# Kernel tuning notes

Measured on AMD Instinct MI355X. Metric: run time of the kernel, lower is better.

## Reference

```python
import jax, jax.numpy as jnp
import numpy as np

EMBED = 1024
HEADS = 16
HEAD_DIM = EMBED // HEADS


def setup_inputs() -> dict:
    key = jax.random.key(0)
    ks = jax.random.split(key, 6)
    s = 1.0 / np.sqrt(EMBED)
    return {
        "x": jax.random.normal(ks[0], (4, 4096, EMBED), dtype=jnp.float32),
        "Wq": jax.random.normal(ks[1], (EMBED, EMBED), dtype=jnp.float32) * s,
        "Wk": jax.random.normal(ks[2], (EMBED, EMBED), dtype=jnp.float32) * s,
        "Wv": jax.random.normal(ks[3], (EMBED, EMBED), dtype=jnp.float32) * s,
        "Wo": jax.random.normal(ks[4], (EMBED, EMBED), dtype=jnp.float32) * s,
        "bo": jax.random.normal(ks[5], (EMBED,), dtype=jnp.float32) * 0.01,
    }


def reference(x, Wq, Wk, Wv, Wo, bo):
    # Faithful to the torch module, including its cross-head attention:
    # the einsum subscripts in the original treat the HEAD axis as the
    # attended (q/k) axis and the SEQUENCE axis as a batch axis.
    N, L, E = x.shape
    H, D = HEADS, HEAD_DIM
    q = (x @ Wq).reshape(N, L, H, D)
    k = (x @ Wk).reshape(N, L, H, D)
    v = (x @ Wv).reshape(N, L, H, D)
    # energy[n, l, hq, hk] = sum_d q[n, l, hq, d] * k[n, l, hk, d]
    energy = jnp.einsum('nlqd,nlkd->nlqk', q, k)  # (N, L, H, H)
    scale = jnp.asarray(E, x.dtype) ** 0.5
    attn = jax.nn.softmax(energy / scale, axis=-1)
    out = jnp.einsum('nlqk,nlkd->nlqd', attn, v).reshape(N, L, E)
    return out @ Wo + bo
```

## Files before the change

### kernel.cpp

```cpp
#include <hip/hip_runtime.h>


typedef unsigned short u16;
typedef unsigned int u32;

typedef __bf16 bf16x8 __attribute__((ext_vector_type(8)));
typedef float f32x4 __attribute__((ext_vector_type(4)));

__device__ __forceinline__ u16 f2bf(float f) {
  u32 u = __float_as_uint(f);
  u += 0x7fffu + ((u >> 16) & 1u);
  return (u16)(u >> 16);
}
__device__ __forceinline__ float bflo(u32 u) { return __uint_as_float(u << 16); }
__device__ __forceinline__ float bfhi(u32 u) { return __uint_as_float(u & 0xffff0000u); }

__device__ __forceinline__ void load_lds16(const u16* g, u16* l) {
  __builtin_amdgcn_global_load_lds(
      (const __attribute__((address_space(1))) u32*)g,
      (__attribute__((address_space(3))) u32*)l, 16, 0, 0);
}

__global__ __launch_bounds__(256) void prep_kernel(
    const float* __restrict__ x, u16* __restrict__ xb,
    const float* __restrict__ Wq, const float* __restrict__ Wk,
    const float* __restrict__ Wv, const float* __restrict__ Wo,
    u16* __restrict__ Wt, u16* __restrict__ Wot) {
  const int bid = blockIdx.x, tid = threadIdx.x;
  if (bid < 8192) {
    size_t i = (size_t)bid * 256 + tid;
    const float4* p = (const float4*)x;
    float4 a = p[2 * i], b = p[2 * i + 1];
    u32 w0 = (u32)f2bf(a.x) | ((u32)f2bf(a.y) << 16);
    u32 w1 = (u32)f2bf(a.z) | ((u32)f2bf(a.w) << 16);
    u32 w2 = (u32)f2bf(b.x) | ((u32)f2bf(b.y) << 16);
    u32 w3 = (u32)f2bf(b.z) | ((u32)f2bf(b.w) << 16);
    *(uint4*)(xb + 8 * i) = make_uint4(w0, w1, w2, w3);
  } else {
    __shared__ float tile[32][33];
    const int b = bid - 8192;
    const int z = b >> 10, rem = b & 1023;
    const float* W = (z == 0) ? Wq : (z == 1) ? Wk : (z == 2) ? Wv : Wo;
    u16* D = (z < 3) ? (Wt + (size_t)z * 1024 * 1024) : Wot;
    const int n0 = (rem & 31) * 32, k0 = (rem >> 5) * 32;
    const int tx = tid & 31, ty = tid >> 5;
#pragma unroll
    for (int i = 0; i < 4; i++)
      tile[ty + i * 8][tx] = W[(size_t)(k0 + ty + i * 8) * 1024 + n0 + tx];
    __syncthreads();
#pragma unroll
    for (int i = 0; i < 4; i++)
      D[(size_t)(n0 + ty + i * 8) * 1024 + k0 + tx] = f2bf(tile[tx][ty + i * 8]);
  }
}


#define SYNC_IN()                                      \
  __builtin_amdgcn_s_barrier();                        \
  asm volatile("s_waitcnt lgkmcnt(0)" ::: "memory");   \
  __builtin_amdgcn_sched_barrier(0)

#define MM(FM, FN, Af, Bf)                                                      \
  do {                                                                          \
    __builtin_amdgcn_s_setprio(1);                                              \
    _Pragma("unroll") for (int m_ = 0; m_ < 4; m_++)                            \
    _Pragma("unroll") for (int j_ = 0; j_ < 2; j_++)                            \
    _Pragma("unroll") for (int k_ = 0; k_ < 2; k_++)                            \
        acc[(FM) + m_][(FN) + j_] = __builtin_amdgcn_mfma_f32_16x16x32_bf16(    \
            Af[m_][k_], Bf[j_][k_], acc[(FM) + m_][(FN) + j_], 0, 0, 0);        \
    __builtin_amdgcn_s_setprio(0);                                              \
  } while (0)

template <int WRITE_MODE>
__global__ __launch_bounds__(512, 2) void gemm8(const u16* __restrict__ A,
                                                const u16* __restrict__ Bt,
                                                void* __restrict__ Cv,
                                                const float* __restrict__ bias,
                                                int N, int K) {
  extern __shared__ __align__(16) u16 smem[];
  const int t = threadIdx.x;
  const int lane = t & 63;
  const int wave = t >> 6;
  const int wm = wave >> 2;
  const int wn = wave & 3;
  const int lrow = lane & 15, lq = lane >> 4;
  const int wm64 = wm * 64, wn32 = wn * 32;

  const int bid = blockIdx.x;
  const int bm_t = ((bid & 7) << 3) | ((bid >> 3) & 7);
  const int bn_t = bid >> 6;
  const size_t bm = (size_t)bm_t * 256;
  const size_t bn = (size_t)bn_t * 256;

  const u16* Ap = A + bm * K;
  const u16* Bp = Bt + bn * K;
  const size_t halfK = (size_t)128 * K;
  const int NT = K >> 6;

  int srow[2], soff[2], sdst[2];
#pragma unroll
  for (int i = 0; i < 2; i++) {
    const int s = (i << 9) + t;
    srow[i] = s >> 3;
    soff[i] = ((s & 7) ^ (srow[i] & 7)) << 3;
    sdst[i] = s << 3;
  }

#define RG(buf, op, h) (smem + ((((buf) << 2) | ((op) << 1) | (h)) << 13))

  auto STG = [&](const u16* Gp, int kt, u16* L) {
#pragma unroll
    for (int i = 0; i < 2; i++)
      load_lds16(Gp + (size_t)srow[i] * K + (kt << 6) + soff[i], L + sdst[i]);
  };
  auto LDA = [&](bf16x8 (&f)[4][2], const u16* base) {
#pragma unroll
    for (int m = 0; m < 4; m++) {
      const int rh = wm64 + m * 16 + lrow;
      const int ro = rh << 6, rx = rh & 7;
#pragma unroll
      for (int ks = 0; ks < 2; ks++)
        f[m][ks] = *(const bf16x8*)&base[ro + ((((ks << 2) + lq) ^ rx) << 3)];
    }
  };
  auto LDB = [&](bf16x8 (&f)[2][2], const u16* base) {
#pragma unroll
    for (int j = 0; j < 2; j++) {
      const int ch = wn32 + j * 16 + lrow;
      const int co = ch << 6, cx = ch & 7;
#pragma unroll
      for (int ks = 0; ks < 2; ks++)
        f[j][ks] = *(const bf16x8*)&base[co + ((((ks << 2) + lq) ^ cx) << 3)];
    }
  };

  f32x4 acc[8][4];
#pragma unroll
  for (int i = 0; i < 8; i++)
#pragma unroll
    for (int j = 0; j < 4; j++) acc[i][j] = 0.0f;

  bf16x8 af[4][2], bf0[2][2], bf1[2][2];

  STG(Ap, 0, RG(0, 0, 0));
  STG(Bp, 0, RG(0, 1, 0));
  STG(Bp + halfK, 0, RG(0, 1, 1));
  STG(Ap + halfK, 0, RG(0, 0, 1));
  STG(Ap, 1, RG(1, 0, 0));
  STG(Bp, 1, RG(1, 1, 0));
  STG(Bp + halfK, 1, RG(1, 1, 1));
  asm volatile("s_waitcnt vmcnt(0)" ::: "memory");
  __builtin_amdgcn_s_barrier();

  for (int tt = 0; tt < NT; ++tt) {
    const int p = tt & 1;
    int t1 = tt + 1; if (t1 >= NT) t1 -= NT;
    int t2 = tt + 2; if (t2 >= NT) t2 -= NT;
    const int q1 = p ^ 1, q2 = p;

    LDA(af, RG(p, 0, 0));
    LDB(bf0, RG(p, 1, 0));
    STG(Ap + halfK, t1, RG(q1, 0, 1));
    SYNC_IN();
    MM(0, 0, af, bf0);
    __builtin_amdgcn_s_barrier();

    LDB(bf1, RG(p, 1, 1));
    STG(Ap, t2, RG(q2, 0, 0));
    SYNC_IN();
    MM(0, 2, af, bf1);
    __builtin_amdgcn_s_barrier();

    LDA(af, RG(p, 0, 1));
    STG(Bp, t2, RG(q2, 1, 0));
    SYNC_IN();
    MM(4, 2, af, bf1);
    __builtin_amdgcn_s_barrier();

    STG(Bp + halfK, t2, RG(q2, 1, 1));
    SYNC_IN();
    MM(4, 0, af, bf0);
    asm volatile("s_waitcnt vmcnt(6)" ::: "memory");
    __builtin_amdgcn_s_barrier();
  }
  asm volatile("s_waitcnt vmcnt(0)" ::: "memory");

#pragma unroll
  for (int fm = 0; fm < 8; fm++) {
    const int MH = fm >> 2, fmr = fm & 3;
#pragma unroll
    for (int fn = 0; fn < 4; fn++) {
      const int NH = fn >> 1, fnr = fn & 1;
      const size_t col = bn + NH * 128 + wn32 + fnr * 16 + lrow;
#pragma unroll
      for (int r = 0; r < 4; r++) {
        const size_t row = bm + MH * 128 + wm64 + fmr * 16 + lq * 4 + r;
        if (WRITE_MODE == 0)
          ((u16*)Cv)[row * N + col] = f2bf(acc[fm][fn][r]);
        else
          ((float*)Cv)[row * N + col] = acc[fm][fn][r] + bias[col];
      }
    }
  }
#undef RG
}

__device__ __forceinline__ void load16f(const u16* p, float* f) {
  const uint4* u = (const uint4*)p;
  uint4 a = u[0], b = u[1];
  f[0] = bflo(a.x);  f[1] = bfhi(a.x);  f[2] = bflo(a.y);  f[3] = bfhi(a.y);
  f[4] = bflo(a.z);  f[5] = bfhi(a.z);  f[6] = bflo(a.w);  f[7] = bfhi(a.w);
  f[8] = bflo(b.x);  f[9] = bfhi(b.x);  f[10] = bflo(b.y); f[11] = bfhi(b.y);
  f[12] = bflo(b.z); f[13] = bfhi(b.z); f[14] = bflo(b.w); f[15] = bfhi(b.w);
}

__global__ __launch_bounds__(256) void attn_kernel(const u16* __restrict__ QKV,
                                                   u16* __restrict__ AO) {
  __shared__ u16 kv[4][2048];
  const int t = threadIdx.x, lane = t & 63, wave = t >> 6;
  const int sub = lane & 3;
  const int tok = blockIdx.x * 4 + wave;

  const u16* base = QKV + (size_t)tok * 3072;
  uint4 k0 = ((const uint4*)(base + 1024))[2 * lane];
  uint4 k1 = ((const uint4*)(base + 1024))[2 * lane + 1];
  uint4 v0 = ((const uint4*)(base + 2048))[2 * lane];
  uint4 v1 = ((const uint4*)(base + 2048))[2 * lane + 1];
  float qf[16];
  load16f(base + lane * 16, qf);
  ((uint4*)&kv[wave][0])[2 * lane] = k0;
  ((uint4*)&kv[wave][0])[2 * lane + 1] = k1;
  ((uint4*)&kv[wave][1024])[2 * lane] = v0;
  ((uint4*)&kv[wave][1024])[2 * lane + 1] = v1;

  float e[16];
#pragma unroll
  for (int hk = 0; hk < 16; hk++) {
    float kf[16];
    load16f(&kv[wave][hk * 64 + sub * 16], kf);
    float s = 0.f;
#pragma unroll
    for (int i = 0; i < 16; i++) s = fmaf(qf[i], kf[i], s);
    s += __shfl_xor(s, 1);
    s += __shfl_xor(s, 2);
    e[hk] = s;
  }

  float m = e[0];
#pragma unroll
  for (int hk = 1; hk < 16; hk++) m = fmaxf(m, e[hk]);
  float sum = 0.f;
#pragma unroll
  for (int hk = 0; hk < 16; hk++) {
    float p = __expf((e[hk] - m) * 0.03125f);
    e[hk] = p;
    sum += p;
  }
  float inv = 1.0f / sum;

  float o[16];
#pragma unroll
  for (int i = 0; i < 16; i++) o[i] = 0.f;
#pragma unroll
  for (int hk = 0; hk < 16; hk++) {
    float a = e[hk] * inv;
    float vf[16];
    load16f(&kv[wave][1024 + hk * 64 + sub * 16], vf);
#pragma unroll
    for (int i = 0; i < 16; i++) o[i] = fmaf(a, vf[i], o[i]);
  }

  u32 w[8];
#pragma unroll
  for (int i = 0; i < 8; i++)
    w[i] = (u32)f2bf(o[2 * i]) | ((u32)f2bf(o[2 * i + 1]) << 16);
  uint4* dst = (uint4*)(AO + (size_t)tok * 1024 + lane * 16);
  dst[0] = make_uint4(w[0], w[1], w[2], w[3]);
  dst[1] = make_uint4(w[4], w[5], w[6], w[7]);
}


extern "C" void kernel_launch(void* const* d_in, const int* in_sizes, int n_in,
                              void* d_out, int out_size, void* d_ws, size_t ws_size,
                              hipStream_t stream) {
  const float* x = (const float*)d_in[0];
  const float* Wq = (const float*)d_in[1];
  const float* Wk = (const float*)d_in[2];
  const float* Wv = (const float*)d_in[3];
  const float* Wo = (const float*)d_in[4];
  const float* bo = (const float*)d_in[5];
  float* out = (float*)d_out;

  char* ws = (char*)d_ws;
  u16* Xb  = (u16*)(ws);
  u16* Wt  = (u16*)(ws + 33554432);
  u16* Wot = (u16*)(ws + 39845888);
  u16* QKV = (u16*)(ws + 41943040);
  u16* AO  = (u16*)(ws + 142606336);

  hipFuncSetAttribute(reinterpret_cast<const void*>(&gemm8<0>),
                      hipFuncAttributeMaxDynamicSharedMemorySize, 131072);
  hipFuncSetAttribute(reinterpret_cast<const void*>(&gemm8<1>),
                      hipFuncAttributeMaxDynamicSharedMemorySize, 131072);

  prep_kernel<<<12288, 256, 0, stream>>>(x, Xb, Wq, Wk, Wv, Wo, Wt, Wot);
  gemm8<0><<<768, 512, 131072, stream>>>(Xb, Wt, QKV, nullptr, 3072, 1024);
  attn_kernel<<<4096, 256, 0, stream>>>(QKV, AO);
  gemm8<1><<<256, 512, 131072, stream>>>(AO, Wot, out, bo, 1024, 1024);
}
```

Measured before the change: 299.5 us.

## Make QKV GEMM blocks persistent over three output tiles with continuous prefetch

The QKV projection GEMM now launches 256 blocks, and each one computes three consecutive 256-wide N tiles for its M tile. The software pipeline keeps prefetching across tile boundaries, so the next tile's B loads overlap the current tile's epilogue. K is also made a compile-time constant. This is meant to cut the tail-wave imbalance of 768 blocks on the CUs and the per-block pipeline fill cost, and to reuse the A tile across N tiles. In exchange, only 256 blocks run, which may underfill a 256-CU device at 2 blocks per CU, and the epilogue stores are serialized inside each block.

Result: no change. 297.7 us (-0.6%).

```diff
diff --git a/kernel.cpp b/kernel.cpp
--- a/kernel.cpp
+++ b/kernel.cpp
@@ -71,12 +71,13 @@
     __builtin_amdgcn_s_setprio(0);                                              \
   } while (0)
 
-template <int WRITE_MODE>
+template <int WRITE_MODE, int OT>
 __global__ __launch_bounds__(512, 2) void gemm8(const u16* __restrict__ A,
                                                 const u16* __restrict__ Bt,
                                                 void* __restrict__ Cv,
                                                 const float* __restrict__ bias,
-                                                int N, int K) {
+                                                int N) {
+  constexpr int K = 1024, NT = 16;
   extern __shared__ __align__(16) u16 smem[];
   const int t = threadIdx.x;
   const int lane = t & 63;
@@ -87,15 +88,19 @@
   const int wm64 = wm * 64, wn32 = wn * 32;
 
   const int bid = blockIdx.x;
-  const int bm_t = ((bid & 7) << 3) | ((bid >> 3) & 7);
-  const int bn_t = bid >> 6;
+  int bm_t, bn0;
+  if (OT == 3) {
+    const int j = bid >> 3;
+    bm_t = ((bid & 7) << 3) | (j >> 2);
+    bn0 = (j & 3) * 3;
+  } else {
+    bm_t = ((bid & 7) << 3) | ((bid >> 3) & 7);
+    bn0 = bid >> 6;
+  }
   const size_t bm = (size_t)bm_t * 256;
-  const size_t bn = (size_t)bn_t * 256;
 
   const u16* Ap = A + bm * K;
-  const u16* Bp = Bt + bn * K;
   const size_t halfK = (size_t)128 * K;
-  const int NT = K >> 6;
 
   int srow[2], soff[2], sdst[2];
 #pragma unroll
@@ -142,64 +147,86 @@
 
   bf16x8 af[4][2], bf0[2][2], bf1[2][2];
 
-  STG(Ap, 0, RG(0, 0, 0));
-  STG(Bp, 0, RG(0, 1, 0));
-  STG(Bp + halfK, 0, RG(0, 1, 1));
-  STG(Ap + halfK, 0, RG(0, 0, 1));
-  STG(Ap, 1, RG(1, 0, 0));
-  STG(Bp, 1, RG(1, 1, 0));
-  STG(Bp + halfK, 1, RG(1, 1, 1));
+  {
+    const u16* Bp0 = Bt + (size_t)bn0 * 256 * K;
+    STG(Ap, 0, RG(0, 0, 0));
+    STG(Bp0, 0, RG(0, 1, 0));
+    STG(Bp0 + halfK, 0, RG(0, 1, 1));
+    STG(Ap + halfK, 0, RG(0, 0, 1));
+    STG(Ap, 1, RG(1, 0, 0));
+    STG(Bp0, 1, RG(1, 1, 0));
+    STG(Bp0 + halfK, 1, RG(1, 1, 1));
+  }
   asm volatile("s_waitcnt vmcnt(0)" ::: "memory");
   __builtin_amdgcn_s_barrier();
 
-  for (int tt = 0; tt < NT; ++tt) {
-    const int p = tt & 1;
-    int t1 = tt + 1; if (t1 >= NT) t1 -= NT;
-    int t2 = tt + 2; if (t2 >= NT) t2 -= NT;
-    const int q1 = p ^ 1, q2 = p;
-
-    LDA(af, RG(p, 0, 0));
-    LDB(bf0, RG(p, 1, 0));
-    STG(Ap + halfK, t1, RG(q1, 0, 1));
-    SYNC_IN();
-    MM(0, 0, af, bf0);
-    __builtin_amdgcn_s_barrier();
-
-    LDB(bf1, RG(p, 1, 1));
-    STG(Ap, t2, RG(q2, 0, 0));
-    SYNC_IN();
-    MM(0, 2, af, bf1);
-    __builtin_amdgcn_s_barrier();
-
-    LDA(af, RG(p, 0, 1));
-    STG(Bp, t2, RG(q2, 1, 0));
-    SYNC_IN();
-    MM(4, 2, af, bf1);
-    __builtin_amdgcn_s_barrier();
-
-    STG(Bp + halfK, t2, RG(q2, 1, 1));
-    SYNC_IN();
-    MM(4, 0, af, bf0);
-    asm volatile("s_waitcnt vmcnt(6)" ::: "memory");
-    __builtin_amdgcn_s_barrier();
-  }
-  asm volatile("s_waitcnt vmcnt(0)" ::: "memory");
-
-#pragma unroll
-  for (int fm = 0; fm < 8; fm++) {
-    const int MH = fm >> 2, fmr = fm & 3;
-#pragma unroll
-    for (int fn = 0; fn < 4; fn++) {
-      const int NH = fn >> 1, fnr = fn & 1;
-      const size_t col = bn + NH * 128 + wn32 + fnr * 16 + lrow;
-#pragma unroll
-      for (int r = 0; r < 4; r++) {
-        const size_t row = bm + MH * 128 + wm64 + fmr * 16 + lq * 4 + r;
-        if (WRITE_MODE == 0)
-          ((u16*)Cv)[row * N + col] = f2bf(acc[fm][fn][r]);
-        else
-          ((float*)Cv)[row * N + col] = acc[fm][fn][r] + bias[col];
+#pragma unroll 1
+  for (int o = 0; o < OT; ++o) {
+#pragma unroll 2
+    for (int tt = 0; tt < NT; ++tt) {
+      const int st = o * NT + tt;
+      const int p = tt & 1;
+      int s1 = st + 1; if (s1 >= OT * NT) s1 -= NT;
+      int s2 = st + 2; if (s2 >= OT * NT) s2 -= NT;
+      const int t1 = s1 & 15;
+      const int o2 = s2 >> 4, t2 = s2 & 15;
+      const u16* B2 = Bt + (size_t)(bn0 + o2) * 256 * K;
+      const int q1 = p ^ 1, q2 = p;
+
+      LDA(af, RG(p, 0, 0));
+      LDB(bf0, RG(p, 1, 0));
+      STG(Ap + halfK, t1, RG(q1, 0, 1));
+      SYNC_IN();
+      MM(0, 0, af, bf0);
+      __builtin_amdgcn_s_barrier();
+
+      LDB(bf1, RG(p, 1, 1));
+      STG(Ap, t2, RG(q2, 0, 0));
+      SYNC_IN();
+      MM(0, 2, af, bf1);
+      __builtin_amdgcn_s_barrier();
+
+      LDA(af, RG(p, 0, 1));
+      STG(B2, t2, RG(q2, 1, 0));
+      SYNC_IN();
+      MM(4, 2, af, bf1);
+      __builtin_amdgcn_s_barrier();
+
+      STG(B2 + halfK, t2, RG(q2, 1, 1));
+      SYNC_IN();
+      MM(4, 0, af, bf0);
+      asm volatile("s_waitcnt vmcnt(6)" ::: "memory");
+      __builtin_amdgcn_s_barrier();
+    }
+
+    if (o + 1 == OT)
+      asm volatile("s_waitcnt vmcnt(0)" ::: "memory");
+
+    {
+      const size_t bcol = (size_t)(bn0 + o) * 256;
+#pragma unroll
+      for (int fm = 0; fm < 8; fm++) {
+        const int MH = fm >> 2, fmr = fm & 3;
+#pragma unroll
+        for (int fn = 0; fn < 4; fn++) {
+          const int NH = fn >> 1, fnr = fn & 1;
+          const size_t col = bcol + NH * 128 + wn32 + fnr * 16 + lrow;
+#pragma unroll
+          for (int r = 0; r < 4; r++) {
+            const size_t row = bm + MH * 128 + wm64 + fmr * 16 + lq * 4 + r;
+            if (WRITE_MODE == 0)
+              ((u16*)Cv)[row * N + col] = f2bf(acc[fm][fn][r]);
+            else
+              ((float*)Cv)[row * N + col] = acc[fm][fn][r] + bias[col];
+          }
+        }
       }
+    }
+    if (o + 1 < OT) {
+#pragma unroll
+      for (int i = 0; i < 8; i++)
+#pragma unroll
+        for (int j = 0; j < 4; j++) acc[i][j] = 0.0f;
     }
   }
 #undef RG
@@ -298,13 +325,13 @@
   u16* QKV = (u16*)(ws + 41943040);
   u16* AO  = (u16*)(ws + 142606336);
 
-  hipFuncSetAttribute(reinterpret_cast<const void*>(&gemm8<0>),
+  hipFuncSetAttribute(reinterpret_cast<const void*>(&gemm8<0, 3>),
                       hipFuncAttributeMaxDynamicSharedMemorySize, 131072);
-  hipFuncSetAttribute(reinterpret_cast<const void*>(&gemm8<1>),
+  hipFuncSetAttribute(reinterpret_cast<const void*>(&gemm8<1, 1>),
                       hipFuncAttributeMaxDynamicSharedMemorySize, 131072);
 
   prep_kernel<<<12288, 256, 0, stream>>>(x, Xb, Wq, Wk, Wv, Wo, Wt, Wot);
-  gemm8<0><<<768, 512, 131072, stream>>>(Xb, Wt, QKV, nullptr, 3072, 1024);
+  gemm8<0, 3><<<256, 512, 131072, stream>>>(Xb, Wt, QKV, nullptr, 3072);
   attn_kernel<<<4096, 256, 0, stream>>>(QKV, AO);
-  gemm8<1><<<256, 512, 131072, stream>>>(AO, Wot, out, bo, 1024, 1024);
-}
+  gemm8<1, 1><<<256, 512, 131072, stream>>>(AO, Wot, out, bo, 1024);
+}
```
